# Kernel tuning notes

Measured on AMD Instinct MI355X. Metric: run time of the kernel, lower is better.

## Reference

```python
import jax, jax.numpy as jnp
import numpy as np

B, L = 2, 2048
D_MODEL, D_INNER, D_STATE, DT_RANK, D_CONV, DEPTH = 1024, 2048, 16, 64, 4, 2
EPS = 1e-5


def setup_inputs() -> dict:
    key = jax.random.key(0)
    ks = jax.random.split(key, 8)
    rn = lambda k, s, scale=0.02: jax.random.normal(k, s, jnp.float32) * scale
    return {
        "x": jax.random.normal(ks[0], (B, L, D_MODEL), jnp.float32),
        "x_size": L,  # truthiness flag only; unused in the math
        "norm_w": jnp.ones((DEPTH, D_MODEL), jnp.float32),
        "norm_b": jnp.zeros((DEPTH, D_MODEL), jnp.float32),
        "in_proj_w": rn(ks[1], (DEPTH, 2 * D_INNER, D_MODEL)),
        "conv_w": rn(ks[2], (DEPTH, D_INNER, 1, D_CONV), 0.1),
        "conv_b": jnp.zeros((DEPTH, D_INNER), jnp.float32),
        "x_proj_w": rn(ks[3], (DEPTH, DT_RANK + 2 * D_STATE, D_INNER)),
        "dt_proj_w": rn(ks[4], (DEPTH, D_INNER, DT_RANK), 0.1),
        "dt_proj_b": jnp.full((DEPTH, D_INNER), -4.0, jnp.float32),  # softplus -> small dt
        "A_log": jnp.broadcast_to(
            jnp.log(jnp.arange(1, D_STATE + 1, dtype=jnp.float32)), (DEPTH, D_INNER, D_STATE)
        ) + jnp.zeros((DEPTH, D_INNER, D_STATE), jnp.float32),
        "D": jnp.ones((DEPTH, D_INNER), jnp.float32),
        "out_proj_w": rn(ks[5], (DEPTH, D_MODEL, D_INNER)),
    }


def _layernorm(x, w, b):
    mu = x.mean(-1, keepdims=True)
    var = ((x - mu) ** 2).mean(-1, keepdims=True)
    return (x - mu) * jax.lax.rsqrt(var + EPS) * w + b


def _selective_scan(u, dt, A, Bm, Cm, Dp):
    # u, dt: (B, L, di); A: (di, n); Bm, Cm: (B, L, n); Dp: (di,)
    def step(h, inp):
        u_t, dt_t, B_t, C_t = inp  # (B,di), (B,di), (B,n), (B,n)
        dA = jnp.exp(dt_t[..., None] * A)                       # (B, di, n)
        h = dA * h + (dt_t * u_t)[..., None] * B_t[:, None, :]  # (B, di, n)
        y = jnp.einsum('bdn,bn->bd', h, C_t)
        return h, y

    h0 = jnp.zeros((u.shape[0], A.shape[0], A.shape[1]), u.dtype)
    xs = (u.swapaxes(0, 1), dt.swapaxes(0, 1), Bm.swapaxes(0, 1), Cm.swapaxes(0, 1))
    _, ys = jax.lax.scan(step, h0, xs)  # ys: (L, B, di)
    return ys.swapaxes(0, 1) + u * Dp


def _mamba(x, in_proj_w, conv_w, conv_b, x_proj_w, dt_proj_w, dt_proj_b, A_log, Dp, out_proj_w):
    xz = jnp.einsum('bld,ed->ble', x, in_proj_w)  # (B, L, 2*di)
    u, z = jnp.split(xz, 2, axis=-1)
    # causal depthwise conv1d, kernel D_CONV
    uc = jax.lax.conv_general_dilated(
        u.swapaxes(1, 2), conv_w, (1,), [(D_CONV - 1, 0)],
        feature_group_count=D_INNER, dimension_numbers=('NCH', 'OIH', 'NCH'))
    u = jax.nn.silu(uc.swapaxes(1, 2) + conv_b)
    x_dbl = jnp.einsum('bld,ed->ble', u, x_proj_w)
    dt_r, Bm, Cm = jnp.split(x_dbl, [DT_RANK, DT_RANK + D_STATE], axis=-1)
    dt = jax.nn.softplus(jnp.einsum('blr,dr->bld', dt_r, dt_proj_w) + dt_proj_b)
    A = -jnp.exp(A_log)
    y = _selective_scan(u, dt, A, Bm, Cm, Dp)
    y = y * jax.nn.silu(z)
    return jnp.einsum('bld,ed->ble', y, out_proj_w)


def reference(x, x_size, norm_w, norm_b, in_proj_w, conv_w, conv_b, x_proj_w,
              dt_proj_w, dt_proj_b, A_log, D, out_proj_w):
    # BasicLayer passes x_size as `residual` (non-None), so each Block reduces to
    # x <- Mamba(LN(x)); the returned residual is discarded by x = blk(...)[0].
    h = x
    for i in range(DEPTH):
        hn = _layernorm(h, norm_w[i], norm_b[i])
        h = _mamba(hn, in_proj_w[i], conv_w[i], conv_b[i], x_proj_w[i],
                   dt_proj_w[i], dt_proj_b[i], A_log[i], D[i], out_proj_w[i])
    return h
```

## Files before the change

### kernel.cpp

```cpp
#include <hip/hip_runtime.h>
#include <hip/hip_bf16.h>
#include <math.h>

#define BQ 2
#define LQ 2048
#define D_MODEL 1024
#define D_INNER 2048
#define D_STATE 16
#define DT_RANK 64
#define D_CONV 4
#define DEPTH 2
#define NCHUNK 64
#define CHUNK 32
#define XSPLITK 8
#define XKC (D_INNER / XSPLITK)
#define OSK 2

typedef __attribute__((ext_vector_type(8))) short short8v;
typedef __attribute__((ext_vector_type(4))) float f32x4;

__device__ __forceinline__ short f2bf(float f) {
    union { float f; unsigned u; } v; v.f = f;
    unsigned r = v.u + 0x7fffu + ((v.u >> 16) & 1u);
    return (short)(r >> 16);
}

__device__ __forceinline__ float bf2f(unsigned short s) {
    union { unsigned u; float f; } v; v.u = ((unsigned)s) << 16;
    return v.f;
}

__device__ __forceinline__ void async16(void* lds, const void* gp) {
    __builtin_amdgcn_global_load_lds(
        (const __attribute__((address_space(1))) void*)gp,
        (__attribute__((address_space(3))) void*)lds, 16, 0, 0);
}

__device__ __forceinline__ void dA_powers(float e1, float* dA) {
    float e2 = e1 * e1, e4 = e2 * e2, e8 = e4 * e4;
    dA[0] = e1;       dA[1] = e2;       dA[2] = e2 * e1;  dA[3] = e4;
    dA[4] = e4 * e1;  dA[5] = e4 * e2;  dA[6] = e4 * dA[2]; dA[7] = e8;
    dA[8] = e8 * e1;  dA[9] = e8 * e2;  dA[10] = e8 * dA[2]; dA[11] = e8 * e4;
    dA[12] = e8 * dA[4]; dA[13] = e8 * dA[5]; dA[14] = e8 * dA[6]; dA[15] = e8 * e8;
}

__global__ __launch_bounds__(256) void layernorm_kernel(
    const float* __restrict__ x, const float* __restrict__ w,
    const float* __restrict__ b, short* __restrict__ out)
{
    __shared__ float red[8];
    int row = blockIdx.x;
    const float* xr = x + (size_t)row * D_MODEL;
    float v[4];
    float s = 0.f, sq = 0.f;
#pragma unroll
    for (int i = 0; i < 4; ++i) {
        v[i] = xr[threadIdx.x + i * 256];
        s += v[i];
        sq += v[i] * v[i];
    }
#pragma unroll
    for (int off = 32; off; off >>= 1) {
        s += __shfl_down(s, off, 64);
        sq += __shfl_down(sq, off, 64);
    }
    int wid = threadIdx.x >> 6, lane = threadIdx.x & 63;
    if (!lane) { red[wid] = s; red[4 + wid] = sq; }
    __syncthreads();
    s = red[0] + red[1] + red[2] + red[3];
    sq = red[4] + red[5] + red[6] + red[7];
    float mu = s * (1.f / D_MODEL);
    float var = sq * (1.f / D_MODEL) - mu * mu;
    float rstd = rsqrtf(var + 1e-5f);
#pragma unroll
    for (int i = 0; i < 4; ++i) {
        int c = threadIdx.x + i * 256;
        out[(size_t)row * D_MODEL + c] = f2bf((v[i] - mu) * rstd * w[c] + b[c]);
    }
}

__global__ __launch_bounds__(256) void osum_ln_kernel(
    const float* __restrict__ P, const float* __restrict__ w,
    const float* __restrict__ b, short* __restrict__ out)
{
    __shared__ float red[8];
    int row = blockIdx.x;
    const float* p0 = P + (size_t)row * D_MODEL;
    const float* p1 = P + (size_t)BQ * LQ * D_MODEL + (size_t)row * D_MODEL;
    float v[4];
    float s = 0.f, sq = 0.f;
#pragma unroll
    for (int i = 0; i < 4; ++i) {
        int c = threadIdx.x + i * 256;
        v[i] = p0[c] + p1[c];
        s += v[i];
        sq += v[i] * v[i];
    }
#pragma unroll
    for (int off = 32; off; off >>= 1) {
        s += __shfl_down(s, off, 64);
        sq += __shfl_down(sq, off, 64);
    }
    int wid = threadIdx.x >> 6, lane = threadIdx.x & 63;
    if (!lane) { red[wid] = s; red[4 + wid] = sq; }
    __syncthreads();
    s = red[0] + red[1] + red[2] + red[3];
    sq = red[4] + red[5] + red[6] + red[7];
    float mu = s * (1.f / D_MODEL);
    float var = sq * (1.f / D_MODEL) - mu * mu;
    float rstd = rsqrtf(var + 1e-5f);
#pragma unroll
    for (int i = 0; i < 4; ++i) {
        int c = threadIdx.x + i * 256;
        out[(size_t)row * D_MODEL + c] = f2bf((v[i] - mu) * rstd * w[c] + b[c]);
    }
}

__global__ __launch_bounds__(512) void gemm256_bf16_kernel(
    const short* __restrict__ A, const short* __restrict__ W,
    short* __restrict__ C, int M, int N, int K)
{
    __shared__ __align__(16) short lds[65536];
    const int tid = threadIdx.x;
    const int lane = tid & 63;
    const int w = tid >> 6;
    const int wr = w >> 2, wc = w & 3;

    int nbx = N >> 8;
    int nwg = (M >> 8) * nbx;
    int q = nwg >> 3;
    int wg = ((int)blockIdx.x & 7) * q + ((int)blockIdx.x >> 3);
    int bx = wg % nbx, by = wg / nbx;
    int bm = by << 8, bn = bx << 8;

    const int fr = lane & 15;
    const int kl = lane >> 4;
    const int srow = lane >> 3;
    const int schunk = (lane & 7) ^ (srow & 7);

    f32x4 acc[8][4] = {};
    short8v af[4][2], bfA[2][2], bfB[2][2];

    auto STAGE = [&](int isA, int buf, int half, int kt) {
        const short* gp = isA ? A : W;
        int tile0 = isA ? bm : bn;
        int base = (isA ? 0 : 32768) + (buf * 2 + half) * 8192;
        int ko = kt << 6;
#pragma unroll
        for (int s = 0; s < 2; ++s) {
            int row = half * 128 + s * 64 + w * 8 + srow;
            const short* src = gp + (size_t)(tile0 + row) * K + ko + schunk * 8;
            async16(&lds[base + s * 4096 + w * 512], src);
        }
    };

    auto LOAD_A = [&](int buf, int mh) {
        int abase = (buf * 2 + mh) * 8192;
#pragma unroll
        for (int i = 0; i < 4; ++i) {
            int rl = wr * 64 + i * 16 + fr;
            int rsw = rl & 7;
#pragma unroll
            for (int ks = 0; ks < 2; ++ks)
                af[i][ks] = *(const short8v*)&lds[abase + rl * 64 + (((ks * 4 + kl) ^ rsw) * 8)];
        }
    };
    auto LOAD_B = [&](int buf, int nh, short8v (&bf)[2][2]) {
        int bbase = 32768 + (buf * 2 + nh) * 8192;
#pragma unroll
        for (int j = 0; j < 2; ++j) {
            int rl = wc * 32 + j * 16 + fr;
            int rsw = rl & 7;
#pragma unroll
            for (int ks = 0; ks < 2; ++ks)
                bf[j][ks] = *(const short8v*)&lds[bbase + rl * 64 + (((ks * 4 + kl) ^ rsw) * 8)];
        }
    };
    auto MFMA_Q = [&](int mh, int nh, short8v (&bf)[2][2]) {
        __builtin_amdgcn_s_setprio(1);
#pragma unroll
        for (int i = 0; i < 4; ++i)
#pragma unroll
            for (int j = 0; j < 2; ++j)
#pragma unroll
                for (int ks = 0; ks < 2; ++ks)
                    acc[mh * 4 + i][nh * 2 + j] = __builtin_amdgcn_mfma_f32_16x16x32_bf16(
                        af[i][ks], bf[j][ks], acc[mh * 4 + i][nh * 2 + j], 0, 0, 0);
        __builtin_amdgcn_s_setprio(0);
    };

#define GBAR  __builtin_amdgcn_s_barrier(); __builtin_amdgcn_sched_barrier(0);
#define LGKM  asm volatile("s_waitcnt lgkmcnt(0)" ::: "memory"); __builtin_amdgcn_sched_barrier(0);

    STAGE(1, 0, 0, 0); STAGE(0, 0, 0, 0);
    STAGE(1, 0, 1, 0); STAGE(0, 0, 1, 0);
    STAGE(1, 1, 0, 1); STAGE(0, 1, 0, 1);

    int T = K >> 7;
    for (int t = 0; t < T; ++t) {
        int last = (t == T - 1);
        asm volatile("s_waitcnt vmcnt(4)" ::: "memory");
        STAGE(1, 1, 1, 2 * t + 1);
        GBAR;
        LOAD_A(0, 0); LOAD_B(0, 0, bfA);
        LGKM; MFMA_Q(0, 0, bfA);
        GBAR;
        STAGE(0, 1, 1, 2 * t + 1);
        GBAR;
        LOAD_B(0, 1, bfB);
        LGKM; MFMA_Q(0, 1, bfB);
        GBAR;
        if (!last) STAGE(1, 0, 0, 2 * t + 2);
        GBAR;
        LOAD_A(0, 1);
        LGKM; MFMA_Q(1, 1, bfB);
        GBAR;
        if (!last) STAGE(0, 0, 0, 2 * t + 2);
        GBAR;
        MFMA_Q(1, 0, bfA);
        GBAR;
        if (last) { asm volatile("s_waitcnt vmcnt(0)" ::: "memory"); }
        else      { asm volatile("s_waitcnt vmcnt(4)" ::: "memory"); }
        if (!last) STAGE(1, 0, 1, 2 * t + 2);
        GBAR;
        LOAD_A(1, 0); LOAD_B(1, 0, bfA);
        LGKM; MFMA_Q(0, 0, bfA);
        GBAR;
        if (!last) STAGE(0, 0, 1, 2 * t + 2);
        GBAR;
        LOAD_B(1, 1, bfB);
        LGKM; MFMA_Q(0, 1, bfB);
        GBAR;
        if (!last) STAGE(1, 1, 0, 2 * t + 3);
        GBAR;
        LOAD_A(1, 1);
        LGKM; MFMA_Q(1, 1, bfB);
        GBAR;
        if (!last) STAGE(0, 1, 0, 2 * t + 3);
        GBAR;
        MFMA_Q(1, 0, bfA);
        GBAR;
    }
#undef GBAR
#undef LGKM

    int cr = (lane >> 4) * 4, cc = lane & 15;
#pragma unroll
    for (int i8 = 0; i8 < 8; ++i8) {
        int mh = i8 >> 2, ii = i8 & 3;
        int row0 = bm + mh * 128 + wr * 64 + ii * 16 + cr;
#pragma unroll
        for (int p = 0; p < 4; ++p) {
            short* Cp = C + (size_t)(row0 + p) * N + bn;
#pragma unroll
            for (int j4 = 0; j4 < 4; ++j4) {
                int nh = j4 >> 1, jj = j4 & 1;
                Cp[nh * 128 + wc * 32 + jj * 16 + cc] = f2bf(acc[i8][j4][p]);
            }
        }
    }
}

__global__ __launch_bounds__(256) void gemm_bf16_kernel(
    const short* __restrict__ A, const short* __restrict__ W,
    void* __restrict__ Cv, int M, int N, int K,
    const float* __restrict__ bias, int epilogue, int nsk)
{
    __shared__ __align__(16) short As[2][128 * 64];
    __shared__ __align__(16) short Bs[2][128 * 64];
    int tid = threadIdx.x;
    int lane = tid & 63, wv = tid >> 6;
    int nbx = N >> 7;
    int nwg = (M >> 7) * nbx;
    int ntot = nwg * nsk;
    int q = ntot >> 3;
    int wgz = ((int)blockIdx.x & 7) * q + ((int)blockIdx.x >> 3);
    int sk = wgz / nwg;
    int wg = wgz % nwg;
    int bx = wg % nbx, by = wg / nbx;
    int bm = by * 128, bn = bx * 128;
    int wr = wv >> 1, wc = wv & 1;
    int Kl = K / nsk;
    int koff = sk * Kl;

    const int fr = lane & 15;
    const int kl = lane >> 4;
    const int srow = lane >> 3;
    const int schunk = (lane & 7) ^ (srow & 7);

    f32x4 acc[4][4] = {};

    const short* Ab = A + (size_t)bm * K + koff;
    const short* Bb = W + (size_t)bn * K + koff;

    auto STAGE = [&](int buf, int kt) {
        int ko = kt << 6;
#pragma unroll
        for (int s = 0; s < 4; ++s) {
            int row = s * 32 + wv * 8 + srow;
            async16(&As[buf][s * 2048 + wv * 512], Ab + (size_t)row * K + ko + schunk * 8);
            async16(&Bs[buf][s * 2048 + wv * 512], Bb + (size_t)row * K + ko + schunk * 8);
        }
    };

    int NT = Kl >> 6;
    STAGE(0, 0);
    if (NT > 1) STAGE(1, 1);

    for (int t = 0; t < NT; ++t) {
        if (t + 1 < NT) { asm volatile("s_waitcnt vmcnt(8)" ::: "memory"); }
        else            { asm volatile("s_waitcnt vmcnt(0)" ::: "memory"); }
        __builtin_amdgcn_s_barrier();
        __builtin_amdgcn_sched_barrier(0);
        int buf = t & 1;
        short8v af[4][2], bf[4][2];
#pragma unroll
        for (int i = 0; i < 4; ++i) {
            int rl = wr * 64 + i * 16 + fr;
            int rsw = rl & 7;
#pragma unroll
            for (int ks = 0; ks < 2; ++ks)
                af[i][ks] = *(const short8v*)&As[buf][rl * 64 + (((ks * 4 + kl) ^ rsw) * 8)];
        }
#pragma unroll
        for (int j = 0; j < 4; ++j) {
            int rl = wc * 64 + j * 16 + fr;
            int rsw = rl & 7;
#pragma unroll
            for (int ks = 0; ks < 2; ++ks)
                bf[j][ks] = *(const short8v*)&Bs[buf][rl * 64 + (((ks * 4 + kl) ^ rsw) * 8)];
        }
        asm volatile("s_waitcnt lgkmcnt(0)" ::: "memory");
        __builtin_amdgcn_sched_barrier(0);
        __builtin_amdgcn_s_setprio(1);
#pragma unroll
        for (int i = 0; i < 4; ++i)
#pragma unroll
            for (int j = 0; j < 4; ++j)
#pragma unroll
                for (int ks = 0; ks < 2; ++ks)
                    acc[i][j] = __builtin_amdgcn_mfma_f32_16x16x32_bf16(
                        af[i][ks], bf[j][ks], acc[i][j], 0, 0, 0);
        __builtin_amdgcn_s_setprio(0);
        __builtin_amdgcn_s_barrier();
        __builtin_amdgcn_sched_barrier(0);
        if (t + 2 < NT) STAGE(buf, t + 2);
    }

    int cr = (lane >> 4) * 4, cc = lane & 15;
    size_t skoff = (size_t)sk * M * N;
#pragma unroll
    for (int i = 0; i < 4; ++i)
#pragma unroll
        for (int p = 0; p < 4; ++p) {
            int row = bm + wr * 64 + i * 16 + cr + p;
#pragma unroll
            for (int j = 0; j < 4; ++j) {
                int col = bn + wc * 64 + cc + j * 16;
                float v = acc[i][j][p];
                if (epilogue == 2)
                    ((short*)Cv)[(size_t)row * N + col] = f2bf(v);
                else
                    ((float*)Cv)[skoff + (size_t)row * N + col] = v;
            }
        }
}

__global__ __launch_bounds__(256) void osum_kernel(
    const float* __restrict__ P, float* __restrict__ out)
{
    size_t i = ((size_t)blockIdx.x * 256 + threadIdx.x) * 4;
    float4 a = *(const float4*)(P + i);
    float4 b = *(const float4*)(P + (size_t)BQ * LQ * D_MODEL + i);
    a.x += b.x; a.y += b.y; a.z += b.z; a.w += b.w;
    *(float4*)(out + i) = a;
}

__global__ __launch_bounds__(256) void dtproj_kernel(
    const short* __restrict__ A, const short* __restrict__ W,
    const float* __restrict__ bias, short* __restrict__ Out)
{
    int lane = threadIdx.x & 63, w = threadIdx.x >> 6;
    int m0 = blockIdx.y * 64 + w * 16;
    int bn = blockIdx.x * 128;
    int fr = lane & 15, fk = (lane >> 4) * 8;
    const short* Ap = A + (size_t)(m0 + fr) * DT_RANK + fk;
    short8v a0 = *(const short8v*)(Ap);
    short8v a1 = *(const short8v*)(Ap + 32);
    f32x4 acc[8] = {};
#pragma unroll
    for (int j = 0; j < 8; ++j) {
        const short* Wp = W + (size_t)(bn + j * 16 + fr) * DT_RANK + fk;
        short8v b0 = *(const short8v*)(Wp);
        short8v b1 = *(const short8v*)(Wp + 32);
        acc[j] = __builtin_amdgcn_mfma_f32_16x16x32_bf16(a0, b0, acc[j], 0, 0, 0);
        acc[j] = __builtin_amdgcn_mfma_f32_16x16x32_bf16(a1, b1, acc[j], 0, 0, 0);
    }
    int cr = (lane >> 4) * 4, cc = lane & 15;
#pragma unroll
    for (int j = 0; j < 8; ++j) {
        int col = bn + j * 16 + cc;
        float bv = bias[col];
#pragma unroll
        for (int p = 0; p < 4; ++p) {
            float v = acc[j][p] + bv;
            v = (v > 20.f) ? v : __logf(1.f + __expf(v));
            Out[(size_t)(m0 + cr + p) * D_INNER + col] = f2bf(v);
        }
    }
}

__global__ __launch_bounds__(256) void xproj_kernel(
    const short* __restrict__ A, const short* __restrict__ W,
    float* __restrict__ Xpart)
{
    int lane = threadIdx.x & 63, wv = threadIdx.x >> 6;
    int sk = blockIdx.x;
    int m0 = blockIdx.y * 64 + wv * 16;
    int fr = lane & 15, fk = (lane >> 4) * 8;
    const short* Ap = A + (size_t)(m0 + fr) * D_INNER + sk * XKC + fk;
    const short* Wp = W + (size_t)fr * D_INNER + sk * XKC + fk;
    f32x4 acc[6] = {};
    for (int k = 0; k < XKC; k += 32) {
        short8v af = *(const short8v*)(Ap + k);
#pragma unroll
        for (int j = 0; j < 6; ++j) {
            short8v bf = *(const short8v*)(Wp + (size_t)j * 16 * D_INNER + k);
            acc[j] = __builtin_amdgcn_mfma_f32_16x16x32_bf16(af, bf, acc[j], 0, 0, 0);
        }
    }
    int cr = (lane >> 4) * 4, cc = lane & 15;
    float* Op = Xpart + ((size_t)sk * (BQ * LQ) + m0 + cr) * 96 + cc;
#pragma unroll
    for (int j = 0; j < 6; ++j)
#pragma unroll
        for (int p = 0; p < 4; ++p)
            Op[(size_t)p * 96 + j * 16] = acc[j][p];
}

__global__ __launch_bounds__(256) void xreduce_kernel(
    const float* __restrict__ Xpart, float* __restrict__ xdbl,
    short* __restrict__ dtr)
{
    size_t i = (size_t)blockIdx.x * 256 + threadIdx.x;
    float s = 0.f;
#pragma unroll
    for (int sk = 0; sk < XSPLITK; ++sk)
        s += Xpart[(size_t)sk * ((size_t)BQ * LQ * 96) + i];
    xdbl[i] = s;
    int col = (int)(i % 96);
    if (col < DT_RANK)
        dtr[(i / 96) * DT_RANK + col] = f2bf(s);
}

__global__ __launch_bounds__(256) void conv_silu_kernel(
    const unsigned short* __restrict__ uz, short* __restrict__ outb,
    const float* __restrict__ w, const float* __restrict__ bias)
{
    int idx = blockIdx.x * 256 + threadIdx.x;
    int e0 = idx * 2;
    int c = e0 & (D_INNER - 1);
    int bl = e0 / D_INNER;
    int l = bl & (LQ - 1);
    int b = bl / LQ;
    float acc0 = bias[c], acc1 = bias[c + 1];
    float w0[D_CONV], w1[D_CONV];
#pragma unroll
    for (int k = 0; k < D_CONV; ++k) {
        w0[k] = w[c * D_CONV + k];
        w1[k] = w[(c + 1) * D_CONV + k];
    }
#pragma unroll
    for (int k = 0; k < D_CONV; ++k) {
        int ls = l - (D_CONV - 1) + k;
        if (ls >= 0) {
            unsigned v = *(const unsigned*)&uz[((size_t)b * LQ + ls) * (2 * D_INNER) + c];
            acc0 += bf2f((unsigned short)(v & 0xffff)) * w0[k];
            acc1 += bf2f((unsigned short)(v >> 16)) * w1[k];
        }
    }
    float v0 = acc0 / (1.f + __expf(-acc0));
    float v1 = acc1 / (1.f + __expf(-acc1));
    unsigned o = (unsigned)(unsigned short)f2bf(v0) |
                 ((unsigned)(unsigned short)f2bf(v1) << 16);
    *(unsigned*)&outb[e0] = o;
}

__global__ __launch_bounds__(256) void scan_phase1_kernel(
    const unsigned short* __restrict__ u, const unsigned short* __restrict__ dt,
    const float* __restrict__ xdbl, const float* __restrict__ A_log,
    float* __restrict__ dtsumb, float* __restrict__ Fbuf)
{
    __shared__ float S[CHUNK][D_STATE];
    int t = threadIdx.x;
    int d = blockIdx.x * 256 + t;
    int c = blockIdx.y;
    int b = blockIdx.z;
    int l0 = c * CHUNK;
    {
        int row = t >> 3, cc2 = (t & 7) * 2;
        const float* src = xdbl + ((size_t)(b * LQ + l0 + row)) * 96 + DT_RANK + cc2;
        *(float2*)&S[row][cc2] = *(const float2*)src;
    }
    float A[D_STATE], h[D_STATE];
    {
        const float4* ap = (const float4*)(A_log + (size_t)d * D_STATE);
#pragma unroll
        for (int g = 0; g < 4; ++g) {
            float4 a = ap[g];
            A[g*4+0] = -__expf(a.x); A[g*4+1] = -__expf(a.y);
            A[g*4+2] = -__expf(a.z); A[g*4+3] = -__expf(a.w);
        }
    }
    bool pf = true;
#pragma unroll
    for (int n = 1; n < D_STATE; ++n)
        pf = pf && (fabsf(A[n] - (float)(n + 1) * A[0]) <= 1e-4f * (float)(n + 1));
#pragma unroll
    for (int n = 0; n < D_STATE; ++n) h[n] = 0.f;
    float dtsum = 0.f;
    float A0 = A[0];
    const unsigned short* up  = u  + ((size_t)b * LQ + l0) * D_INNER + d;
    const unsigned short* dtp = dt + ((size_t)b * LQ + l0) * D_INNER + d;
    __syncthreads();

    if (pf) {
        for (int lb = 0; lb < CHUNK; lb += 8) {
            float uvv[8], dtvv[8];
#pragma unroll
            for (int i = 0; i < 8; ++i) {
                uvv[i]  = bf2f(up [(size_t)(lb + i) * D_INNER]);
                dtvv[i] = bf2f(dtp[(size_t)(lb + i) * D_INNER]);
            }
#pragma unroll
            for (int i = 0; i < 8; ++i) {
                int l = lb + i;
                float dtv = dtvv[i];
                float du = dtv * uvv[i];
                dtsum += dtv;
                float dA[D_STATE];
                dA_powers(__expf(dtv * A0), dA);
#pragma unroll
                for (int n4 = 0; n4 < D_STATE; n4 += 4) {
                    float4 Bv = *(const float4*)&S[l][n4];
                    float bb[4] = {Bv.x, Bv.y, Bv.z, Bv.w};
#pragma unroll
                    for (int k = 0; k < 4; ++k) {
                        int n = n4 + k;
                        h[n] = dA[n] * h[n] + du * bb[k];
                    }
                }
            }
        }
    } else {
        for (int lb = 0; lb < CHUNK; lb += 8) {
            float uvv[8], dtvv[8];
#pragma unroll
            for (int i = 0; i < 8; ++i) {
                uvv[i]  = bf2f(up [(size_t)(lb + i) * D_INNER]);
                dtvv[i] = bf2f(dtp[(size_t)(lb + i) * D_INNER]);
            }
#pragma unroll
            for (int i = 0; i < 8; ++i) {
                int l = lb + i;
                float dtv = dtvv[i];
                float du = dtv * uvv[i];
                dtsum += dtv;
#pragma unroll
                for (int n4 = 0; n4 < D_STATE; n4 += 4) {
                    float4 Bv = *(const float4*)&S[l][n4];
                    float bb[4] = {Bv.x, Bv.y, Bv.z, Bv.w};
#pragma unroll
                    for (int k = 0; k < 4; ++k) {
                        int n = n4 + k;
                        float dA = __expf(dtv * A[n]);
                        h[n] = dA * h[n] + du * bb[k];
                    }
                }
            }
        }
    }
    dtsumb[(size_t)(b * NCHUNK + c) * D_INNER + d] = dtsum;
    size_t base = ((size_t)(b * NCHUNK + c) * D_STATE) * D_INNER + d;
#pragma unroll
    for (int n = 0; n < D_STATE; ++n)
        Fbuf[base + (size_t)n * D_INNER] = h[n];
}

__global__ __launch_bounds__(256) void scan_phase2_kernel(
    const float* __restrict__ dtsumb, const float* __restrict__ A_log,
    float* __restrict__ Fbuf)
{
    int d = blockIdx.x * 256 + threadIdx.x;
    int n = blockIdx.y;
    int b = blockIdx.z;
    float A = -__expf(A_log[(size_t)d * D_STATE + n]);
    float hinit = 0.f;
    for (int c = 0; c < NCHUNK; ++c) {
        size_t idx = ((size_t)(b * NCHUNK + c) * D_STATE + n) * D_INNER + d;
        float F = Fbuf[idx];
        float P = __expf(A * dtsumb[(size_t)(b * NCHUNK + c) * D_INNER + d]);
        Fbuf[idx] = hinit;
        hinit = P * hinit + F;
    }
}

__global__ __launch_bounds__(256) void scan_phase3_kernel(
    const unsigned short* __restrict__ u, const unsigned short* __restrict__ dt,
    const float* __restrict__ xdbl, const float* __restrict__ A_log,
    const float* __restrict__ Dp, const float* __restrict__ Hinit,
    const unsigned short* __restrict__ uz, short* __restrict__ yout)
{
    __shared__ float S[CHUNK][32];
    int t = threadIdx.x;
    int d = blockIdx.x * 256 + t;
    int c = blockIdx.y;
    int b = blockIdx.z;
    int l0 = c * CHUNK;
    {
        int row = t >> 3, cg = (t & 7) * 4;
        const float* src = xdbl + ((size_t)(b * LQ + l0 + row)) * 96 + DT_RANK + cg;
        *(float4*)&S[row][cg ^ ((row & 7) << 2)] = *(const float4*)src;
    }
    float A[D_STATE], h[D_STATE];
    {
        const float4* ap = (const float4*)(A_log + (size_t)d * D_STATE);
#pragma unroll
        for (int g = 0; g < 4; ++g) {
            float4 a = ap[g];
            A[g*4+0] = -__expf(a.x); A[g*4+1] = -__expf(a.y);
            A[g*4+2] = -__expf(a.z); A[g*4+3] = -__expf(a.w);
        }
    }
    bool pf = true;
#pragma unroll
    for (int n = 1; n < D_STATE; ++n)
        pf = pf && (fabsf(A[n] - (float)(n + 1) * A[0]) <= 1e-4f * (float)(n + 1));
    size_t base = ((size_t)(b * NCHUNK + c) * D_STATE) * D_INNER + d;
#pragma unroll
    for (int n = 0; n < D_STATE; ++n)
        h[n] = Hinit[base + (size_t)n * D_INNER];
    float Dd = Dp[d];
    float A0 = A[0];
    const unsigned short* up  = u  + ((size_t)b * LQ + l0) * D_INNER + d;
    const unsigned short* dtp = dt + ((size_t)b * LQ + l0) * D_INNER + d;
    const unsigned short* zp = uz + ((size_t)b * LQ + l0) * (2 * D_INNER) + D_INNER + d;
    short* yp = yout + ((size_t)b * LQ + l0) * D_INNER + d;
    __syncthreads();

    if (pf) {
        for (int lb = 0; lb < CHUNK; lb += 8) {
            float uvv[8], dtvv[8], zvv[8];
#pragma unroll
            for (int i = 0; i < 8; ++i) {
                uvv[i]  = bf2f(up [(size_t)(lb + i) * D_INNER]);
                dtvv[i] = bf2f(dtp[(size_t)(lb + i) * D_INNER]);
                zvv[i]  = bf2f(zp [(size_t)(lb + i) * (2 * D_INNER)]);
            }
#pragma unroll
            for (int i = 0; i < 8; ++i) {
                int l = lb + i;
                float dtv = dtvv[i];
                float du = dtv * uvv[i];
                float acc = 0.f;
                int sw = (l & 7) << 2;
                float dA[D_STATE];
                dA_powers(__expf(dtv * A0), dA);
#pragma unroll
                for (int n4 = 0; n4 < D_STATE; n4 += 4) {
                    float4 Bv = *(const float4*)&S[l][n4 ^ sw];
                    float4 Cv = *(const float4*)&S[l][(16 + n4) ^ sw];
                    float bb[4] = {Bv.x, Bv.y, Bv.z, Bv.w};
                    float cc[4] = {Cv.x, Cv.y, Cv.z, Cv.w};
#pragma unroll
                    for (int k = 0; k < 4; ++k) {
                        int n = n4 + k;
                        h[n] = dA[n] * h[n] + du * bb[k];
                        acc += h[n] * cc[k];
                    }
                }
                float y = acc + uvv[i] * Dd;
                float zv = zvv[i];
                float g = zv / (1.f + __expf(-zv));
                yp[(size_t)l * D_INNER] = f2bf(y * g);
            }
        }
    } else {
        for (int lb = 0; lb < CHUNK; lb += 8) {
            float uvv[8], dtvv[8], zvv[8];
#pragma unroll
            for (int i = 0; i < 8; ++i) {
                uvv[i]  = bf2f(up [(size_t)(lb + i) * D_INNER]);
                dtvv[i] = bf2f(dtp[(size_t)(lb + i) * D_INNER]);
                zvv[i]  = bf2f(zp [(size_t)(lb + i) * (2 * D_INNER)]);
            }
#pragma unroll
            for (int i = 0; i < 8; ++i) {
                int l = lb + i;
                float dtv = dtvv[i];
                float du = dtv * uvv[i];
                float acc = 0.f;
                int sw = (l & 7) << 2;
#pragma unroll
                for (int n4 = 0; n4 < D_STATE; n4 += 4) {
                    float4 Bv = *(const float4*)&S[l][n4 ^ sw];
                    float4 Cv = *(const float4*)&S[l][(16 + n4) ^ sw];
                    float bb[4] = {Bv.x, Bv.y, Bv.z, Bv.w};
                    float cc[4] = {Cv.x, Cv.y, Cv.z, Cv.w};
#pragma unroll
                    for (int k = 0; k < 4; ++k) {
                        int n = n4 + k;
                        float dA = __expf(dtv * A[n]);
                        h[n] = dA * h[n] + du * bb[k];
                        acc += h[n] * cc[k];
                    }
                }
                float y = acc + uvv[i] * Dd;
                float zv = zvv[i];
                float g = zv / (1.f + __expf(-zv));
                yp[(size_t)l * D_INNER] = f2bf(y * g);
            }
        }
    }
}

__global__ __launch_bounds__(256) void convert_all_kernel(
    const float* __restrict__ w_in, const float* __restrict__ w_out,
    const float* __restrict__ w_xp, const float* __restrict__ w_dt,
    short* __restrict__ wbuf)
{
    const int IN_B  = (2 * D_INNER * D_MODEL) / 1024;
    const int OUT_B = (D_MODEL * D_INNER) / 1024;
    const int XP_B  = (96 * D_INNER) / 1024;
    int blk = blockIdx.x;
    const float* src; short* dst;
    if (blk < IN_B)                 { src = w_in;  dst = wbuf; }
    else if (blk < IN_B + OUT_B)    { src = w_out; dst = wbuf + 2 * D_INNER * D_MODEL; blk -= IN_B; }
    else if (blk < IN_B + OUT_B + XP_B) { src = w_xp; dst = wbuf + 2 * D_INNER * D_MODEL + D_MODEL * D_INNER; blk -= IN_B + OUT_B; }
    else { src = w_dt; dst = wbuf + 2 * D_INNER * D_MODEL + D_MODEL * D_INNER + 96 * D_INNER; blk -= IN_B + OUT_B + XP_B; }
    int i = blk * 1024 + threadIdx.x * 4;
    float4 v = *(const float4*)(src + i);
    short4 o = make_short4(f2bf(v.x), f2bf(v.y), f2bf(v.z), f2bf(v.w));
    *(short4*)(dst + i) = o;
}

extern "C" void kernel_launch(void* const* d_in, const int* in_sizes, int n_in,
                              void* d_out, int out_size, void* d_ws, size_t ws_size,
                              hipStream_t stream)
{
    const float* x        = (const float*)d_in[0];
    const float* norm_w   = (const float*)d_in[2];
    const float* norm_b   = (const float*)d_in[3];
    const float* in_proj  = (const float*)d_in[4];
    const float* conv_w   = (const float*)d_in[5];
    const float* conv_b   = (const float*)d_in[6];
    const float* x_proj   = (const float*)d_in[7];
    const float* dt_proj  = (const float*)d_in[8];
    const float* dt_projb = (const float*)d_in[9];
    const float* A_log    = (const float*)d_in[10];
    const float* Dp       = (const float*)d_in[11];
    const float* out_proj = (const float*)d_in[12];
    float* out = (float*)d_out;
    float* ws  = (float*)d_ws;

    const size_t BL   = (size_t)BQ * LQ;
    const size_t BLDM = BL * D_MODEL;
    const size_t BLDI = BL * D_INNER;
    const int IN_W  = 2 * D_INNER * D_MODEL;
    const int OUT_W = D_MODEL * D_INNER;
    const int XP_W  = 96 * D_INNER;
    const int DT_W  = D_INNER * DT_RANK;
    const int CV_BLOCKS = (IN_W + OUT_W + XP_W + DT_W) / 1024;

    size_t o = 0;
    short* hnb   = (short*)(ws + o); o += BLDM / 2;
    short* uzb   = (short*)(ws + o); o += BL * 2 * D_INNER / 2;
    short* dtb   = (short*)(ws + o); o += BLDI / 2;
    float* xdbl  = ws + o; o += BL * 96;
    float* Xpart = ws + o; o += (size_t)XSPLITK * BL * 96;
    float* Fbuf  = ws + o; o += (size_t)BQ * NCHUNK * D_STATE * D_INNER;
    float* dtsumb = ws + o; o += (size_t)BQ * NCHUNK * D_INNER;
    short* ucx   = (short*)(ws + o); o += BLDI / 2;
    short* dtr   = (short*)(ws + o); o += BL * DT_RANK / 2;
    float* Opart = ws + o; o += (size_t)OSK * BLDM;
    short* wbuf  = (short*)(ws + o);
    o += (size_t)(IN_W + OUT_W + XP_W + DT_W + 1) / 2;

    for (int layer = 0; layer < DEPTH; ++layer) {
        if (layer == 0)
            layernorm_kernel<<<(int)BL, 256, 0, stream>>>(
                x, norm_w, norm_b, hnb);

        convert_all_kernel<<<CV_BLOCKS, 256, 0, stream>>>(
            in_proj + (size_t)layer * IN_W, out_proj + (size_t)layer * OUT_W,
            x_proj + (size_t)layer * XP_W, dt_proj + (size_t)layer * DT_W, wbuf);

        gemm256_bf16_kernel<<<(int)(BL / 256) * (2 * D_INNER / 256), 512, 0, stream>>>(
            hnb, wbuf, uzb, (int)BL, 2 * D_INNER, D_MODEL);

        conv_silu_kernel<<<(int)(BLDI / 512), 256, 0, stream>>>(
            (const unsigned short*)uzb, ucx,
            conv_w + (size_t)layer * D_INNER * D_CONV,
            conv_b + (size_t)layer * D_INNER);

        xproj_kernel<<<dim3(XSPLITK, BL / 64), 256, 0, stream>>>(
            ucx, wbuf + IN_W + OUT_W, Xpart);
        xreduce_kernel<<<(int)(BL * 96 / 256), 256, 0, stream>>>(Xpart, xdbl, dtr);

        dtproj_kernel<<<dim3(D_INNER / 128, BL / 64), 256, 0, stream>>>(
            dtr, wbuf + IN_W + OUT_W + XP_W,
            dt_projb + (size_t)layer * D_INNER, dtb);

        const float* Al = A_log + (size_t)layer * D_INNER * D_STATE;
        scan_phase1_kernel<<<dim3(D_INNER / 256, NCHUNK, BQ), 256, 0, stream>>>(
            (const unsigned short*)ucx, (const unsigned short*)dtb, xdbl, Al,
            dtsumb, Fbuf);
        scan_phase2_kernel<<<dim3(D_INNER / 256, D_STATE, BQ), 256, 0, stream>>>(
            dtsumb, Al, Fbuf);
        scan_phase3_kernel<<<dim3(D_INNER / 256, NCHUNK, BQ), 256, 0, stream>>>(
            (const unsigned short*)ucx, (const unsigned short*)dtb, xdbl, Al,
            Dp + (size_t)layer * D_INNER, Fbuf,
            (const unsigned short*)uzb, (short*)ucx);

        gemm_bf16_kernel<<<(int)(BL / 128) * (D_MODEL / 128) * OSK, 256, 0, stream>>>(
            ucx, wbuf + IN_W, Opart, (int)BL, D_MODEL, D_INNER, nullptr, 0, OSK);

        if (layer == DEPTH - 1)
            osum_kernel<<<(int)(BLDM / 1024), 256, 0, stream>>>(Opart, out);
        else
            osum_ln_kernel<<<(int)BL, 256, 0, stream>>>(
                Opart, norm_w + (size_t)(layer + 1) * D_MODEL,
                norm_b + (size_t)(layer + 1) * D_MODEL, hnb);
    }
}
```

Measured before the change: 430.8 us.

## Double-buffer scan phase-3 u/dt/z loads through LDS with async copies

The phase-3 scan kernel now stages its u, dt and z bf16 rows into double-buffered shared memory with 16-byte async global-to-LDS copies, prefetching the next 8-step block while the current one is computed. This replaces per-thread strided 2-byte global loads and is meant to hide memory latency behind the serial recurrence. It adds two block barriers per 8-step block, extra LDS, and relies on hand-written waitcnt counts matching the async16 helper.

```diff
diff --git a/kernel.cpp b/kernel.cpp
--- a/kernel.cpp
+++ b/kernel.cpp
@@ -612,8 +612,12 @@
     const unsigned short* __restrict__ uz, short* __restrict__ yout)
 {
     __shared__ float S[CHUNK][32];
+    __shared__ __align__(16) unsigned short Ub[2][8][256];
+    __shared__ __align__(16) unsigned short Db[2][8][256];
+    __shared__ __align__(16) unsigned short Zb[2][8][256];
     int t = threadIdx.x;
-    int d = blockIdx.x * 256 + t;
+    int d0 = blockIdx.x * 256;
+    int d = d0 + t;
     int c = blockIdx.y;
     int b = blockIdx.z;
     int l0 = c * CHUNK;
@@ -622,6 +626,19 @@
         const float* src = xdbl + ((size_t)(b * LQ + l0 + row)) * 96 + DT_RANK + cg;
         *(float4*)&S[row][cg ^ ((row & 7) << 2)] = *(const float4*)src;
     }
+    const int w = t >> 6, lane = t & 63;
+    const int srw = 2 * w + (lane >> 5);
+    const int scl = (lane & 31) * 8;
+    const unsigned short* ubp = u  + ((size_t)b * LQ + l0) * D_INNER + d0;
+    const unsigned short* dbp = dt + ((size_t)b * LQ + l0) * D_INNER + d0;
+    const unsigned short* zbp = uz + ((size_t)b * LQ + l0) * (2 * D_INNER) + D_INNER + d0;
+    auto STAGE3 = [&](int buf, int lb) {
+        async16(&Ub[buf][2 * w][0], ubp + (size_t)(lb + srw) * D_INNER + scl);
+        async16(&Db[buf][2 * w][0], dbp + (size_t)(lb + srw) * D_INNER + scl);
+        async16(&Zb[buf][2 * w][0], zbp + (size_t)(lb + srw) * (2 * D_INNER) + scl);
+    };
+    STAGE3(0, 0);
+
     float A[D_STATE], h[D_STATE];
     {
         const float4* ap = (const float4*)(A_log + (size_t)d * D_STATE);
@@ -642,24 +659,30 @@
         h[n] = Hinit[base + (size_t)n * D_INNER];
     float Dd = Dp[d];
     float A0 = A[0];
-    const unsigned short* up  = u  + ((size_t)b * LQ + l0) * D_INNER + d;
-    const unsigned short* dtp = dt + ((size_t)b * LQ + l0) * D_INNER + d;
-    const unsigned short* zp = uz + ((size_t)b * LQ + l0) * (2 * D_INNER) + D_INNER + d;
     short* yp = yout + ((size_t)b * LQ + l0) * D_INNER + d;
-    __syncthreads();
-
-    if (pf) {
-        for (int lb = 0; lb < CHUNK; lb += 8) {
-            float uvv[8], dtvv[8], zvv[8];
+    asm volatile("s_waitcnt lgkmcnt(0)" ::: "memory");
+
+    for (int bb = 0; bb < CHUNK / 8; ++bb) {
+        int buf = bb & 1;
+        if (bb + 1 < CHUNK / 8) {
+            STAGE3(buf ^ 1, (bb + 1) * 8);
+            asm volatile("s_waitcnt vmcnt(3)" ::: "memory");
+        } else {
+            asm volatile("s_waitcnt vmcnt(0)" ::: "memory");
+        }
+        __builtin_amdgcn_s_barrier();
+        __builtin_amdgcn_sched_barrier(0);
+        float uvv[8], dtvv[8], zvv[8];
+#pragma unroll
+        for (int i = 0; i < 8; ++i) {
+            uvv[i]  = bf2f(Ub[buf][i][t]);
+            dtvv[i] = bf2f(Db[buf][i][t]);
+            zvv[i]  = bf2f(Zb[buf][i][t]);
+        }
+        if (pf) {
 #pragma unroll
             for (int i = 0; i < 8; ++i) {
-                uvv[i]  = bf2f(up [(size_t)(lb + i) * D_INNER]);
-                dtvv[i] = bf2f(dtp[(size_t)(lb + i) * D_INNER]);
-                zvv[i]  = bf2f(zp [(size_t)(lb + i) * (2 * D_INNER)]);
-            }
-#pragma unroll
-            for (int i = 0; i < 8; ++i) {
-                int l = lb + i;
+                int l = bb * 8 + i;
                 float dtv = dtvv[i];
                 float du = dtv * uvv[i];
                 float acc = 0.f;
@@ -670,13 +693,13 @@
                 for (int n4 = 0; n4 < D_STATE; n4 += 4) {
                     float4 Bv = *(const float4*)&S[l][n4 ^ sw];
                     float4 Cv = *(const float4*)&S[l][(16 + n4) ^ sw];
-                    float bb[4] = {Bv.x, Bv.y, Bv.z, Bv.w};
-                    float cc[4] = {Cv.x, Cv.y, Cv.z, Cv.w};
+                    float bb2[4] = {Bv.x, Bv.y, Bv.z, Bv.w};
+                    float cc2[4] = {Cv.x, Cv.y, Cv.z, Cv.w};
 #pragma unroll
                     for (int k = 0; k < 4; ++k) {
                         int n = n4 + k;
-                        h[n] = dA[n] * h[n] + du * bb[k];
-                        acc += h[n] * cc[k];
+                        h[n] = dA[n] * h[n] + du * bb2[k];
+                        acc += h[n] * cc2[k];
                     }
                 }
                 float y = acc + uvv[i] * Dd;
@@ -684,19 +707,10 @@
                 float g = zv / (1.f + __expf(-zv));
                 yp[(size_t)l * D_INNER] = f2bf(y * g);
             }
-        }
-    } else {
-        for (int lb = 0; lb < CHUNK; lb += 8) {
-            float uvv[8], dtvv[8], zvv[8];
+        } else {
 #pragma unroll
             for (int i = 0; i < 8; ++i) {
-                uvv[i]  = bf2f(up [(size_t)(lb + i) * D_INNER]);
-                dtvv[i] = bf2f(dtp[(size_t)(lb + i) * D_INNER]);
-                zvv[i]  = bf2f(zp [(size_t)(lb + i) * (2 * D_INNER)]);
-            }
-#pragma unroll
-            for (int i = 0; i < 8; ++i) {
-                int l = lb + i;
+                int l = bb * 8 + i;
                 float dtv = dtvv[i];
                 float du = dtv * uvv[i];
                 float acc = 0.f;
@@ -705,14 +719,14 @@
                 for (int n4 = 0; n4 < D_STATE; n4 += 4) {
                     float4 Bv = *(const float4*)&S[l][n4 ^ sw];
                     float4 Cv = *(const float4*)&S[l][(16 + n4) ^ sw];
-                    float bb[4] = {Bv.x, Bv.y, Bv.z, Bv.w};
-                    float cc[4] = {Cv.x, Cv.y, Cv.z, Cv.w};
+                    float bb2[4] = {Bv.x, Bv.y, Bv.z, Bv.w};
+                    float cc2[4] = {Cv.x, Cv.y, Cv.z, Cv.w};
 #pragma unroll
                     for (int k = 0; k < 4; ++k) {
                         int n = n4 + k;
                         float dA = __expf(dtv * A[n]);
-                        h[n] = dA * h[n] + du * bb[k];
-                        acc += h[n] * cc[k];
+                        h[n] = dA * h[n] + du * bb2[k];
+                        acc += h[n] * cc2[k];
                     }
                 }
                 float y = acc + uvv[i] * Dd;
@@ -721,6 +735,8 @@
                 yp[(size_t)l * D_INNER] = f2bf(y * g);
             }
         }
+        __builtin_amdgcn_s_barrier();
+        __builtin_amdgcn_sched_barrier(0);
     }
 }
 
```

Measured after the change: 405.3 us. 5.9% less time.
